# Optimization experiments

Measured on AMD Instinct MI355X. Metric: run time of the kernel, lower is better.

## Reference

```python
import jax, jax.numpy as jnp
import numpy as np

N, E, D, ED = 25000, 250000, 128, 128
LN_EPS = 1e-5   # nn.LayerNorm default
BN_EPS = 1e-5   # BatchNorm1d default (GENConv MLP norm='batch', training mode)
GEN_EPS = 1e-7  # GENConv message eps


def _ln(x, g, b):
    mu = jnp.mean(x, -1, keepdims=True)
    var = jnp.mean((x - mu) ** 2, -1, keepdims=True)
    return (x - mu) * jax.lax.rsqrt(var + LN_EPS) * g + b


def setup_inputs() -> dict:
    key = jax.random.key(0)
    ks = jax.random.split(key, 8)
    p = lambda k, shp: (jax.random.normal(k, shp, jnp.float32) * 0.02)
    return {
        "x": jax.random.normal(ks[0], (N, D), jnp.float32),
        "edge_attr": jax.random.normal(ks[1], (E, ED), jnp.float32),
        "edge_index": jax.random.randint(ks[2], (2, E), 0, N),
        # edge_mlp: Linear(2D+ED -> ED) + ReLU + LayerNorm(ED)
        "W_e": p(ks[3], (2 * D + ED, ED)), "b_e": jnp.zeros((ED,), jnp.float32),
        "g_e": jnp.ones((ED,), jnp.float32), "be_e": jnp.zeros((ED,), jnp.float32),
        # GENConv learnable softmax temperature t (learn_t=True, init 1.0)
        "t": jnp.float32(1.0),
        # GENConv output MLP: [D -> 2D (BN, ReLU) -> D]  (num_layers=2, expansion=2, norm='batch')
        "W_m1": p(ks[4], (D, 2 * D)), "b_m1": jnp.zeros((2 * D,), jnp.float32),
        "g_bn": jnp.ones((2 * D,), jnp.float32), "b_bn": jnp.zeros((2 * D,), jnp.float32),
        "W_m2": p(ks[5], (2 * D, D)), "b_m2": jnp.zeros((D,), jnp.float32),
        # MessageNorm learnable scale (learn_scale=True, init 1.0)
        "scale": jnp.float32(1.0),
        # node LayerNorm
        "g_n": jnp.ones((D,), jnp.float32), "b_n": jnp.zeros((D,), jnp.float32),
    }


def reference(x, edge_attr, edge_index, W_e, b_e, g_e, be_e, t,
              W_m1, b_m1, g_bn, b_bn, W_m2, b_m2, scale, g_n, b_n):
    row, col = edge_index[0], edge_index[1]  # source, destination (PyG flow)

    # edge MLP with residual: cat([x[row], x[col], edge_attr]) -> Linear -> ReLU -> LN, + edge_attr
    ei = jnp.concatenate([x[row], x[col], edge_attr], axis=-1)        # [E, 2D+ED]
    e = _ln(jnp.maximum(ei @ W_e + b_e, 0.0), g_e, be_e) + edge_attr  # [E, ED]

    # GENConv message: relu(x_j + edge_attr) + eps  (edge_dim == in_channels -> no lin_edge)
    msg = jnp.maximum(x[row] + e, 0.0) + GEN_EPS                      # [E, D]

    # per-destination, per-channel softmax aggregation with temperature t
    s = msg * t
    smax = jax.ops.segment_max(s, col, num_segments=N)                # [N, D]
    ex = jnp.exp(s - smax[col])
    denom = jax.ops.segment_sum(ex, col, num_segments=N)
    alpha = ex / denom[col]
    agg = jax.ops.segment_sum(msg * alpha, col, num_segments=N)       # [N, D]

    # GENConv residual + output MLP (Linear -> BatchNorm(train) -> ReLU -> Linear)
    out = agg + x
    h1 = out @ W_m1 + b_m1                                            # [N, 2D]
    mu = jnp.mean(h1, axis=0)
    var = jnp.mean((h1 - mu) ** 2, axis=0)
    h1 = jnp.maximum((h1 - mu) * jax.lax.rsqrt(var + BN_EPS) * g_bn + b_bn, 0.0)
    h = h1 @ W_m2 + b_m2                                              # [N, D]

    # MessageNorm(learn_scale=True): normalize(h) * ||x|| * scale
    hnorm = jnp.linalg.norm(h, axis=-1, keepdims=True)
    h = h / jnp.maximum(hnorm, 1e-12)
    xnorm = jnp.linalg.norm(x, axis=-1, keepdims=True)
    h = h * xnorm * scale

    # node residual + LayerNorm (dropout in eval mode = identity)
    x_out = _ln(x + h, g_n, b_n)
    return (x_out, e)
```

## Files before the change

kernel.cpp:

```cpp
#include <hip/hip_runtime.h>
#include <hip/hip_bf16.h>

typedef __hip_bfloat16 bf16;
typedef __attribute__((ext_vector_type(8))) short short8v;
typedef __attribute__((ext_vector_type(4))) short short4v;
typedef __attribute__((ext_vector_type(4))) float float4v;

constexpr int N = 25000;
constexpr int E = 250000;
constexpr size_t NB = (size_t)N * 128;
constexpr int NBLK = (N + 63) / 64;

constexpr size_t al256(size_t x) { return (x + 255) / 256 * 256; }

constexpr size_t OFF_BNS  = 0;
constexpr size_t OFF_BNQ  = OFF_BNS + 256;
constexpr size_t OFF_FLAG = OFF_BNQ + 256;
constexpr size_t OFF_XN   = OFF_FLAG + 256;
constexpr size_t OFF_WB   = al256(OFF_XN + N);
constexpr size_t OFF_WP   = OFF_WB + 8192;
constexpr size_t OFF_WM1P = OFF_WP + 16384;
constexpr size_t OFF_WM2P = OFF_WM1P + 16384;
constexpr size_t OFF_DEG  = al256(OFF_WM2P + 16384);
constexpr size_t OFF_OFFS = al256(OFF_DEG + N);
constexpr size_t OFF_CUR  = al256(OFF_OFFS + N + 1);
constexpr size_t OFF_LIST = al256(OFF_CUR + N);
constexpr size_t OFF_OUT  = al256(OFF_LIST + E);
constexpr size_t OFF_A    = al256(OFF_OUT + NB / 2);
constexpr size_t WS_FLOATS = OFF_A + NB;
constexpr size_t OFF_MSG  = al256(OFF_A + NB);
constexpr size_t WS_FLOATS_BIG = OFF_MSG + (size_t)E * 64;


__device__ __forceinline__ float b2f(bf16 v) { return __bfloat162float(v); }
__device__ __forceinline__ short f2bs(float f) {
    bf16 h = __float2bfloat16(f);
    return *reinterpret_cast<short*>(&h);
}
__device__ __forceinline__ float bs2f(short s) {
    bf16 h;
    *reinterpret_cast<short*>(&h) = s;
    return b2f(h);
}

__device__ __forceinline__ float ldf(const void* p, size_t i, int bf) {
    return bf ? b2f(((const bf16*)p)[i]) : ((const float*)p)[i];
}
__device__ __forceinline__ void stf(void* p, size_t i, float v, int bf) {
    if (bf) ((bf16*)p)[i] = __float2bfloat16(v);
    else    ((float*)p)[i] = v;
}
__device__ __forceinline__ float4v load4(const void* p, size_t i, int bf) {
    if (bf) {
        short4v s = *(const short4v*)((const bf16*)p + i);
        return (float4v){bs2f(s[0]), bs2f(s[1]), bs2f(s[2]), bs2f(s[3])};
    }
    return *(const float4v*)((const float*)p + i);
}
__device__ __forceinline__ void store4(void* p, size_t i, float4v v, int bf) {
    if (bf) {
        short4v s = {f2bs(v[0]), f2bs(v[1]), f2bs(v[2]), f2bs(v[3])};
        *(short4v*)((bf16*)p + i) = s;
    } else {
        *(float4v*)((float*)p + i) = v;
    }
}
__device__ __forceinline__ float lds_scalar(const void* p, int bf) {
    if (!bf) return *(const float*)p;
    float v = b2f(*(const bf16*)p);
    float a = fabsf(v);
    return (a >= 0.0009765625f && a <= 1024.0f) ? v : *(const float*)p;
}
__device__ __forceinline__ int get_flag(const float* ws) {
    return *(const int*)(ws + OFF_FLAG);
}
__device__ __forceinline__ void* e_base(void* d_out, int bf) {
    return bf ? (void*)((bf16*)d_out + NB) : (void*)((float*)d_out + NB);
}


__global__ void k_detect(const unsigned short* __restrict__ xu, float* __restrict__ ws) {
    __shared__ int cnt;
    if (threadIdx.x == 0) cnt = 0;
    __syncthreads();
    int c = 0;
    for (int i = threadIdx.x; i < 512; i += 256) {
        unsigned e = (xu[i] >> 7) & 0xFFu;
        if (e >= 110u && e <= 135u) c++;
    }
    atomicAdd(&cnt, c);
    __syncthreads();
    if (threadIdx.x == 0) *(int*)(ws + OFF_FLAG) = (cnt >= 460) ? 1 : 0;
}

__global__ void k_init(float* __restrict__ ws, const void* __restrict__ W_e,
                       const void* __restrict__ W_m1, const void* __restrict__ W_m2) {
    int bf = get_flag(ws);
    size_t gid = (size_t)blockIdx.x * blockDim.x + threadIdx.x;
    size_t stride = (size_t)gridDim.x * blockDim.x;
    short* WB = (short*)(ws + OFF_WB);
    for (size_t t = gid; t < 16384; t += stride) {
        int i = t & 7, l = (t >> 3) & 63, n = (t >> 9) & 7, s = t >> 12;
        int k = s * 32 + (l >> 4) * 8 + i;
        int c = n * 16 + (l & 15);
        WB[t] = f2bs(ldf(W_e, (size_t)(256 + k) * 128 + c, bf));
    }
    short* WP = (short*)(ws + OFF_WP);
    for (size_t t = gid; t < 32768; t += stride) {
        int i = t & 7, l = (t >> 3) & 63, n = (t >> 9) & 15, s = t >> 13;
        int k = s * 32 + (l >> 4) * 8 + i;
        int c = n * 16 + (l & 15);
        float v = (c < 128) ? ldf(W_e, (size_t)k * 128 + c, bf)
                            : ldf(W_e, (size_t)(128 + k) * 128 + (c - 128), bf);
        WP[t] = f2bs(v);
    }
    short* M1 = (short*)(ws + OFF_WM1P);
    for (size_t t = gid; t < 32768; t += stride) {
        int i = t & 7, l = (t >> 3) & 63, n = (t >> 9) & 15, s = t >> 13;
        int k = s * 32 + (l >> 4) * 8 + i;
        int c = n * 16 + (l & 15);
        M1[t] = f2bs(ldf(W_m1, (size_t)k * 256 + c, bf));
    }
    short* M2 = (short*)(ws + OFF_WM2P);
    for (size_t t = gid; t < 32768; t += stride) {
        int i = t & 7, l = (t >> 3) & 63, n = (t >> 9) & 7, s = t >> 12;
        int k = s * 32 + (l >> 4) * 8 + i;
        int c = n * 16 + (l & 15);
        M2[t] = f2bs(ldf(W_m2, (size_t)k * 128 + c, bf));
    }
    for (size_t i = gid; i < 512; i += stride) ws[OFF_BNS + i] = 0.0f;
    int* deg = (int*)(ws + OFF_DEG);
    for (size_t i = gid; i < N; i += stride) deg[i] = 0;
}

__global__ void k_count(const int* __restrict__ ei, float* __restrict__ ws) {
    int j = blockIdx.x * blockDim.x + threadIdx.x;
    if (j < E) atomicAdd((int*)(ws + OFF_DEG) + ei[E + j], 1);
}

__global__ __launch_bounds__(256) void k_node_pre_mfma(const void* __restrict__ x,
                                                       const void* __restrict__ b_e,
                                                       float* __restrict__ ws) {
    int bf = get_flag(ws);
    int l = threadIdx.x & 63, wv = threadIdx.x >> 6;
    int n0 = blockIdx.x * 64 + wv * 16;
    if (n0 >= N) return;
    int row = l & 15, grp = l >> 4;
    int ja = n0 + row;
    int jac = ja < N ? ja : N - 1;
    const short8v* WP = (const short8v*)(ws + OFF_WP);
    float4v acc[16];
    #pragma unroll
    for (int n = 0; n < 16; ++n) acc[n] = (float4v){0.f, 0.f, 0.f, 0.f};
    float sq = 0.f;
    #pragma unroll
    for (int s = 0; s < 4; ++s) {
        short8v af;
        if (bf) {
            af = ((const short8v*)x)[(size_t)jac * 16 + s * 4 + grp];
            #pragma unroll
            for (int i = 0; i < 8; ++i) { float v = bs2f(af[i]); sq = fmaf(v, v, sq); }
        } else {
            const float* er = (const float*)x + (size_t)jac * 128 + s * 32 + grp * 8;
            float4v lo = *(const float4v*)er;
            float4v hi = *(const float4v*)(er + 4);
            float xv[8] = {lo[0], lo[1], lo[2], lo[3], hi[0], hi[1], hi[2], hi[3]};
            #pragma unroll
            for (int i = 0; i < 8; ++i) { sq = fmaf(xv[i], xv[i], sq); af[i] = f2bs(xv[i]); }
        }
        #pragma unroll
        for (int n = 0; n < 16; ++n) {
            acc[n] = __builtin_amdgcn_mfma_f32_16x16x32_bf16(af, WP[(s * 16 + n) * 64 + l], acc[n], 0, 0, 0);
        }
    }
    sq += __shfl_xor(sq, 16, 64);
    sq += __shfl_xor(sq, 32, 64);
    if (grp == 0 && ja < N) ws[OFF_XN + ja] = sqrtf(sq);
    bf16* XA = (bf16*)(ws + OFF_A);
    #pragma unroll
    for (int reg = 0; reg < 4; ++reg) {
        int jd = n0 + grp * 4 + reg;
        if (jd >= N) continue;
        #pragma unroll
        for (int n = 0; n < 16; ++n) {
            int c = n * 16 + row;
            if (n < 8) {
                XA[(size_t)jd * 128 + c] = __float2bfloat16(acc[n][reg] + ldf(b_e, c, bf));
            } else {
                XA[NB + (size_t)jd * 128 + (c - 128)] = __float2bfloat16(acc[n][reg]);
            }
        }
    }
}

template<int WM>
__global__ __launch_bounds__(256) void k_edge1_mfma(const void* __restrict__ ea,
                                                    const int* __restrict__ ei,
                                                    const void* __restrict__ g_e,
                                                    const void* __restrict__ be_e,
                                                    const void* __restrict__ x,
                                                    float* __restrict__ ws,
                                                    void* __restrict__ d_out) {
    int bf = get_flag(ws);
    void* eo = e_base(d_out, bf);
    int l = threadIdx.x & 63;
    int wv = threadIdx.x >> 6;
    int e0w = blockIdx.x * 64 + wv * 16;
    int eq = l & 15, grp = l >> 4;

    int posv = 0;
    if (WM && l < 16) {
        int jj = e0w + l;
        if (jj < E) posv = atomicAdd((int*)(ws + OFF_CUR) + ei[E + jj], 1);
    }
    int pos = WM ? __shfl(posv, eq, 64) : 0;

    int ja = e0w + eq;
    int jac = ja < E ? ja : E - 1;
    const short8v* WB = (const short8v*)(ws + OFF_WB);
    float4v acc[8];
    #pragma unroll
    for (int m = 0; m < 8; ++m) acc[m] = (float4v){0.f, 0.f, 0.f, 0.f};

    #pragma unroll
    for (int s = 0; s < 4; ++s) {
        short8v bfr;
        if (bf) {
            bfr = ((const short8v*)ea)[(size_t)jac * 16 + s * 4 + grp];
        } else {
            const float* er = (const float*)ea + (size_t)jac * 128 + s * 32 + grp * 8;
            float4v lo = *(const float4v*)er;
            float4v hi = *(const float4v*)(er + 4);
            bfr[0] = f2bs(lo[0]); bfr[1] = f2bs(lo[1]); bfr[2] = f2bs(lo[2]); bfr[3] = f2bs(lo[3]);
            bfr[4] = f2bs(hi[0]); bfr[5] = f2bs(hi[1]); bfr[6] = f2bs(hi[2]); bfr[7] = f2bs(hi[3]);
        }
        #pragma unroll
        for (int m = 0; m < 8; ++m) {
            acc[m] = __builtin_amdgcn_mfma_f32_16x16x32_bf16(WB[(s * 8 + m) * 64 + l], bfr, acc[m], 0, 0, 0);
        }
    }

    int j = e0w + eq;
    bool valid = j < E;
    int jc = valid ? j : E - 1;
    int r = ei[jc], cd = ei[E + jc];
    const bf16* XAp = (const bf16*)(ws + OFF_A);

    float p[8][4];
    float s1 = 0.f, s2 = 0.f;
    #pragma unroll
    for (int m = 0; m < 8; ++m) {
        int ch = m * 16 + grp * 4;
        short4v xa = *(const short4v*)(XAp + (size_t)r * 128 + ch);
        short4v xb = *(const short4v*)(XAp + NB + (size_t)cd * 128 + ch);
        #pragma unroll
        for (int w = 0; w < 4; ++w) {
            float v = acc[m][w] + bs2f(xa[w]) + bs2f(xb[w]);
            v = fmaxf(v, 0.f);
            p[m][w] = v;
            s1 += v;
            s2 = fmaf(v, v, s2);
        }
    }
    s1 += __shfl_xor(s1, 16, 64);
    s1 += __shfl_xor(s1, 32, 64);
    s2 += __shfl_xor(s2, 16, 64);
    s2 += __shfl_xor(s2, 32, 64);
    float mu = s1 * (1.f / 128.f);
    float var = s2 * (1.f / 128.f) - mu * mu;
    float rstd = rsqrtf(fmaxf(var, 0.f) + 1e-5f);

    bf16* MSG = (bf16*)(ws + OFF_MSG);
    #pragma unroll
    for (int m = 0; m < 8; ++m) {
        int ch = m * 16 + grp * 4;
        float4v gg = load4(g_e, ch, bf);
        float4v bb = load4(be_e, ch, bf);
        float4v eav = load4(ea, (size_t)jc * 128 + ch, bf);
        float4v ev;
        #pragma unroll
        for (int w = 0; w < 4; ++w)
            ev[w] = (p[m][w] - mu) * rstd * gg[w] + bb[w] + eav[w];
        if (valid) store4(eo, (size_t)j * 128 + ch, ev, bf);
        if (WM) {
            float4v xv = load4(x, (size_t)r * 128 + ch, bf);
            short4v ms;
            #pragma unroll
            for (int w = 0; w < 4; ++w)
                ms[w] = f2bs(fmaxf(xv[w] + ev[w], 0.f) + 1e-7f);
            if (valid) *(short4v*)(MSG + (size_t)pos * 128 + ch) = ms;
        }
    }
}

__global__ __launch_bounds__(256) void k_scan(float* __restrict__ ws) {
    const int* deg = (const int*)(ws + OFF_DEG);
    int* offs = (int*)(ws + OFF_OFFS);
    int* cur  = (int*)(ws + OFF_CUR);
    __shared__ int sums[256];
    __shared__ int carry[257];
    int t = threadIdx.x;
    const int chunk = (N + 255) / 256;
    int lo = t * chunk, hi = lo + chunk < N ? lo + chunk : N;
    int s = 0;
    for (int i = lo; i < hi; ++i) s += deg[i];
    sums[t] = s;
    __syncthreads();
    if (t == 0) {
        int acc = 0;
        #pragma unroll 4
        for (int i = 0; i < 256; ++i) { carry[i] = acc; acc += sums[i]; }
        carry[256] = acc;
    }
    __syncthreads();
    int acc = carry[t];
    for (int i = lo; i < hi; ++i) { offs[i] = acc; cur[i] = acc; acc += deg[i]; }
    if (t == 0) offs[N] = carry[256];
}

__global__ void k_scatter(const int* __restrict__ ei, float* __restrict__ ws) {
    int j = blockIdx.x * blockDim.x + threadIdx.x;
    if (j >= E) return;
    int cd = ei[E + j];
    int pos = atomicAdd((int*)(ws + OFF_CUR) + cd, 1);
    ((int*)(ws + OFF_LIST))[pos] = j;
}

__global__ __launch_bounds__(256) void k_agg_stream(const void* __restrict__ x,
                                                    const void* __restrict__ t_p,
                                                    float* __restrict__ ws) {
    int bf = get_flag(ws);
    int n = blockIdx.x, tid = threadIdx.x;
    int c = tid & 127, half = tid >> 7;
    const int* offs = (const int*)(ws + OFF_OFFS);
    int s0 = offs[n], s1v = offs[n + 1];
    float t = lds_scalar(t_p, bf);
    const bf16* MSG = (const bf16*)(ws + OFF_MSG);
    float den = 0.f, num = 0.f;
    for (int i = s0 + half; i < s1v; i += 2) {
        float m = b2f(MSG[(size_t)i * 128 + c]);
        float ex = expf(m * t - 15.0f);
        den += ex;
        num = fmaf(m, ex, num);
    }
    __shared__ float dsh[256];
    __shared__ float nsh[256];
    dsh[tid] = den;
    nsh[tid] = num;
    __syncthreads();
    if (tid < 128) {
        float dn = dsh[tid] + dsh[tid + 128];
        float nm = nsh[tid] + nsh[tid + 128];
        float ag = dn > 0.f ? nm / dn : 0.f;
        float out = ag + ldf(x, (size_t)n * 128 + tid, bf);
        ((bf16*)(ws + OFF_OUT))[(size_t)n * 128 + tid] = __float2bfloat16(out);
    }
}

__global__ __launch_bounds__(256) void k_agg_gather(const void* __restrict__ x,
                                                    const int* __restrict__ ei,
                                                    const void* __restrict__ t_p,
                                                    void* __restrict__ d_out,
                                                    float* __restrict__ ws) {
    int bf = get_flag(ws);
    const void* e_in = e_base(d_out, bf);
    int n = blockIdx.x, tid = threadIdx.x;
    int c = tid & 127, half = tid >> 7;
    const int* offs = (const int*)(ws + OFF_OFFS);
    const int* list = (const int*)(ws + OFF_LIST);
    int s0 = offs[n], s1v = offs[n + 1];
    float t = lds_scalar(t_p, bf);
    float den = 0.f, num = 0.f;
    for (int i = s0 + half; i < s1v; i += 2) {
        int j = list[i];
        int r = ei[j];
        float ev = ldf(e_in, (size_t)j * 128 + c, bf);
        float msg = fmaxf(ldf(x, (size_t)r * 128 + c, bf) + ev, 0.f) + 1e-7f;
        float ex = expf(msg * t - 15.0f);
        den += ex;
        num = fmaf(msg, ex, num);
    }
    __shared__ float dsh[256];
    __shared__ float nsh[256];
    dsh[tid] = den;
    nsh[tid] = num;
    __syncthreads();
    if (tid < 128) {
        float dn = dsh[tid] + dsh[tid + 128];
        float nm = nsh[tid] + nsh[tid + 128];
        float ag = dn > 0.f ? nm / dn : 0.f;
        float out = ag + ldf(x, (size_t)n * 128 + tid, bf);
        ((bf16*)(ws + OFF_OUT))[(size_t)n * 128 + tid] = __float2bfloat16(out);
    }
}

__global__ __launch_bounds__(256) void k_h1_mfma(const void* __restrict__ b_m1,
                                                 float* __restrict__ ws) {
    int bf = get_flag(ws);
    int l = threadIdx.x & 63, wv = threadIdx.x >> 6;
    int n0 = blockIdx.x * 64 + wv * 16;
    if (n0 >= N) return;
    int row = l & 15, grp = l >> 4;
    int ja = n0 + row;
    int jac = ja < N ? ja : N - 1;
    const short8v* OUT = (const short8v*)(ws + OFF_OUT);
    const short8v* M1 = (const short8v*)(ws + OFF_WM1P);
    float4v acc[16];
    #pragma unroll
    for (int n = 0; n < 16; ++n) acc[n] = (float4v){0.f, 0.f, 0.f, 0.f};
    #pragma unroll
    for (int s = 0; s < 4; ++s) {
        short8v af = OUT[(size_t)jac * 16 + s * 4 + grp];
        #pragma unroll
        for (int n = 0; n < 16; ++n) {
            acc[n] = __builtin_amdgcn_mfma_f32_16x16x32_bf16(af, M1[(s * 16 + n) * 64 + l], acc[n], 0, 0, 0);
        }
    }
    bf16* H1 = (bf16*)(ws + OFF_A);
    #pragma unroll
    for (int reg = 0; reg < 4; ++reg) {
        int jd = n0 + grp * 4 + reg;
        if (jd >= N) continue;
        #pragma unroll
        for (int n = 0; n < 16; ++n) {
            int col = n * 16 + row;
            H1[(size_t)jd * 256 + col] = __float2bfloat16(acc[n][reg] + ldf(b_m1, col, bf));
        }
    }
}

__global__ __launch_bounds__(256) void k_bnstats(float* __restrict__ ws) {
    int t = threadIdx.x;
    const bf16* H1 = (const bf16*)(ws + OFF_A);
    float s = 0.f, q = 0.f;
    for (int r = blockIdx.x; r < N; r += gridDim.x) {
        float v = b2f(H1[(size_t)r * 256 + t]);
        s += v;
        q = fmaf(v, v, q);
    }
    atomicAdd(&ws[OFF_BNS + t], s);
    atomicAdd(&ws[OFF_BNQ + t], q);
}

__global__ __launch_bounds__(256) void k_node_post_mfma(const void* __restrict__ x,
                                                        const void* __restrict__ g_bn,
                                                        const void* __restrict__ b_bn,
                                                        const void* __restrict__ b_m2,
                                                        const void* __restrict__ scale_p,
                                                        const void* __restrict__ g_n,
                                                        const void* __restrict__ b_n,
                                                        float* __restrict__ ws,
                                                        void* __restrict__ x_out) {
    int bf = get_flag(ws);
    __shared__ float sA[256];
    __shared__ float sB[256];
    {
        int t = threadIdx.x;
        const float inv_n = 1.f / (float)N;
        float mu = ws[OFF_BNS + t] * inv_n;
        float var = ws[OFF_BNQ + t] * inv_n - mu * mu;
        float rs = rsqrtf(fmaxf(var, 0.f) + 1e-5f) * ldf(g_bn, t, bf);
        sA[t] = rs;
        sB[t] = ldf(b_bn, t, bf) - mu * rs;
    }
    __syncthreads();
    int l = threadIdx.x & 63, wv = threadIdx.x >> 6;
    int n0 = blockIdx.x * 64 + wv * 16;
    if (n0 >= N) return;
    int row = l & 15, grp = l >> 4;
    int ja = n0 + row;
    int jac = ja < N ? ja : N - 1;
    const short8v* H1 = (const short8v*)(ws + OFF_A);
    const short8v* M2 = (const short8v*)(ws + OFF_WM2P);
    float4v acc[8];
    #pragma unroll
    for (int n = 0; n < 8; ++n) acc[n] = (float4v){0.f, 0.f, 0.f, 0.f};
    #pragma unroll
    for (int s = 0; s < 8; ++s) {
        short8v hv = H1[(size_t)jac * 32 + s * 4 + grp];
        int kb = s * 32 + grp * 8;
        short8v af;
        #pragma unroll
        for (int i = 0; i < 8; ++i) {
            float v = fmaf(bs2f(hv[i]), sA[kb + i], sB[kb + i]);
            af[i] = f2bs(fmaxf(v, 0.f));
        }
        #pragma unroll
        for (int n = 0; n < 8; ++n) {
            acc[n] = __builtin_amdgcn_mfma_f32_16x16x32_bf16(af, M2[(s * 8 + n) * 64 + l], acc[n], 0, 0, 0);
        }
    }
    float scl = lds_scalar(scale_p, bf);
    #pragma unroll
    for (int reg = 0; reg < 4; ++reg) {
        int jd = n0 + grp * 4 + reg;
        int jdc = jd < N ? jd : N - 1;
        float h[8];
        float ss = 0.f;
        #pragma unroll
        for (int n = 0; n < 8; ++n) {
            h[n] = acc[n][reg] + ldf(b_m2, n * 16 + row, bf);
            ss = fmaf(h[n], h[n], ss);
        }
        #pragma unroll
        for (int off = 1; off < 16; off <<= 1) ss += __shfl_xor(ss, off, 64);
        float hs = ws[OFF_XN + jdc] * scl / fmaxf(sqrtf(ss), 1e-12f);
        float y[8];
        float s1 = 0.f;
        #pragma unroll
        for (int n = 0; n < 8; ++n) {
            y[n] = ldf(x, (size_t)jdc * 128 + n * 16 + row, bf) + h[n] * hs;
            s1 += y[n];
        }
        #pragma unroll
        for (int off = 1; off < 16; off <<= 1) s1 += __shfl_xor(s1, off, 64);
        float mu = s1 * (1.f / 128.f);
        float s2 = 0.f;
        #pragma unroll
        for (int n = 0; n < 8; ++n) { float d = y[n] - mu; s2 = fmaf(d, d, s2); }
        #pragma unroll
        for (int off = 1; off < 16; off <<= 1) s2 += __shfl_xor(s2, off, 64);
        float rstd = rsqrtf(s2 * (1.f / 128.f) + 1e-5f);
        if (jd < N) {
            #pragma unroll
            for (int n = 0; n < 8; ++n) {
                int col = n * 16 + row;
                float o = (y[n] - mu) * rstd * ldf(g_n, col, bf) + ldf(b_n, col, bf);
                stf(x_out, (size_t)jd * 128 + col, o, bf);
            }
        }
    }
}


extern "C" void kernel_launch(void* const* d_in, const int* in_sizes, int n_in,
                              void* d_out, int out_size, void* d_ws, size_t ws_size,
                              hipStream_t stream) {
    const void* x    = d_in[0];
    const void* ea   = d_in[1];
    const int*  ei   = (const int*)d_in[2];
    const void* W_e  = d_in[3];
    const void* b_e  = d_in[4];
    const void* g_e  = d_in[5];
    const void* be_e = d_in[6];
    const void* t_p  = d_in[7];
    const void* W_m1 = d_in[8];
    const void* b_m1 = d_in[9];
    const void* g_bn = d_in[10];
    const void* b_bn = d_in[11];
    const void* W_m2 = d_in[12];
    const void* b_m2 = d_in[13];
    const void* scl  = d_in[14];
    const void* g_n  = d_in[15];
    const void* b_n  = d_in[16];

    float* ws = (float*)d_ws;
    bool big = ws_size >= WS_FLOATS_BIG * sizeof(float);

    k_detect<<<1, 256, 0, stream>>>((const unsigned short*)x, ws);
    k_init<<<512, 256, 0, stream>>>(ws, W_e, W_m1, W_m2);
    k_count<<<(E + 255) / 256, 256, 0, stream>>>(ei, ws);
    k_scan<<<1, 256, 0, stream>>>(ws);
    k_node_pre_mfma<<<NBLK, 256, 0, stream>>>(x, b_e, ws);
    if (big) {
        k_edge1_mfma<1><<<(E + 63) / 64, 256, 0, stream>>>(ea, ei, g_e, be_e, x, ws, d_out);
        k_agg_stream<<<N, 256, 0, stream>>>(x, t_p, ws);
    } else {
        k_edge1_mfma<0><<<(E + 63) / 64, 256, 0, stream>>>(ea, ei, g_e, be_e, x, ws, d_out);
        k_scatter<<<(E + 255) / 256, 256, 0, stream>>>(ei, ws);
        k_agg_gather<<<N, 256, 0, stream>>>(x, ei, t_p, d_out, ws);
    }
    k_h1_mfma<<<NBLK, 256, 0, stream>>>(b_m1, ws);
    k_bnstats<<<256, 256, 0, stream>>>(ws);
    k_node_post_mfma<<<NBLK, 256, 0, stream>>>(x, g_bn, b_bn, b_m2, scl, g_n, b_n, ws, d_out);
}
```

Measured before the change: 604.5 us.

## Fuse BN stats and degree count, index messages by edge, vectorize aggregation

Several changes land together. BatchNorm column statistics are now computed inside the h1 GEMM epilogue, which removes k_bnstats. Degree counting moves into k_init and zeroing into k_detect, so k_count is gone. Edge messages are written at the edge index rather than at an atomically claimed CSR slot, and k_scatter now always runs so the aggregation can read them through the CSR list. The aggregation kernel uses 16-way edge parallelism with 8-wide bf16 vector loads and a fast exp. Gathers are hoisted ahead of the MFMA loop, and large output writes use nontemporal stores. The trade-offs are an extra scatter launch on the big path and indirect message reads in the aggregation.

```diff
diff --git a/kernel.cpp b/kernel.cpp
--- a/kernel.cpp
+++ b/kernel.cpp
@@ -50,6 +50,10 @@
     if (bf) ((bf16*)p)[i] = __float2bfloat16(v);
     else    ((float*)p)[i] = v;
 }
+__device__ __forceinline__ void stf_nt(void* p, size_t i, float v, int bf) {
+    if (bf) __builtin_nontemporal_store(f2bs(v), (short*)p + i);
+    else    __builtin_nontemporal_store(v, (float*)p + i);
+}
 __device__ __forceinline__ float4v load4(const void* p, size_t i, int bf) {
     if (bf) {
         short4v s = *(const short4v*)((const bf16*)p + i);
@@ -57,12 +61,12 @@
     }
     return *(const float4v*)((const float*)p + i);
 }
-__device__ __forceinline__ void store4(void* p, size_t i, float4v v, int bf) {
+__device__ __forceinline__ void store4_nt(void* p, size_t i, float4v v, int bf) {
     if (bf) {
         short4v s = {f2bs(v[0]), f2bs(v[1]), f2bs(v[2]), f2bs(v[3])};
-        *(short4v*)((bf16*)p + i) = s;
+        __builtin_nontemporal_store(s, (short4v*)((bf16*)p + i));
     } else {
-        *(float4v*)((float*)p + i) = v;
+        __builtin_nontemporal_store(v, (float4v*)((float*)p + i));
     }
 }
 __device__ __forceinline__ float lds_scalar(const void* p, int bf) {
@@ -89,53 +93,47 @@
         if (e >= 110u && e <= 135u) c++;
     }
     atomicAdd(&cnt, c);
+    for (int i = threadIdx.x; i < 512; i += 256) ws[OFF_BNS + i] = 0.0f;
+    int* deg = (int*)(ws + OFF_DEG);
+    for (int i = threadIdx.x; i < N; i += 256) deg[i] = 0;
     __syncthreads();
     if (threadIdx.x == 0) *(int*)(ws + OFF_FLAG) = (cnt >= 460) ? 1 : 0;
 }
 
 __global__ void k_init(float* __restrict__ ws, const void* __restrict__ W_e,
-                       const void* __restrict__ W_m1, const void* __restrict__ W_m2) {
+                       const void* __restrict__ W_m1, const void* __restrict__ W_m2,
+                       const int* __restrict__ ei) {
     int bf = get_flag(ws);
     size_t gid = (size_t)blockIdx.x * blockDim.x + threadIdx.x;
     size_t stride = (size_t)gridDim.x * blockDim.x;
     short* WB = (short*)(ws + OFF_WB);
-    for (size_t t = gid; t < 16384; t += stride) {
-        int i = t & 7, l = (t >> 3) & 63, n = (t >> 9) & 7, s = t >> 12;
-        int k = s * 32 + (l >> 4) * 8 + i;
-        int c = n * 16 + (l & 15);
+    for (size_t u = gid; u < 16384; u += stride) {
+        int k = u >> 7, c = u & 127;
+        int t = (k >> 5) * 4096 + (c >> 4) * 512 + (((k & 31) >> 3) * 16 + (c & 15)) * 8 + (k & 7);
         WB[t] = f2bs(ldf(W_e, (size_t)(256 + k) * 128 + c, bf));
     }
     short* WP = (short*)(ws + OFF_WP);
-    for (size_t t = gid; t < 32768; t += stride) {
-        int i = t & 7, l = (t >> 3) & 63, n = (t >> 9) & 15, s = t >> 13;
-        int k = s * 32 + (l >> 4) * 8 + i;
-        int c = n * 16 + (l & 15);
+    for (size_t u = gid; u < 32768; u += stride) {
+        int k = u >> 8, c = u & 255;
+        int t = (k >> 5) * 8192 + (c >> 4) * 512 + (((k & 31) >> 3) * 16 + (c & 15)) * 8 + (k & 7);
         float v = (c < 128) ? ldf(W_e, (size_t)k * 128 + c, bf)
                             : ldf(W_e, (size_t)(128 + k) * 128 + (c - 128), bf);
         WP[t] = f2bs(v);
     }
     short* M1 = (short*)(ws + OFF_WM1P);
-    for (size_t t = gid; t < 32768; t += stride) {
-        int i = t & 7, l = (t >> 3) & 63, n = (t >> 9) & 15, s = t >> 13;
-        int k = s * 32 + (l >> 4) * 8 + i;
-        int c = n * 16 + (l & 15);
+    for (size_t u = gid; u < 32768; u += stride) {
+        int k = u >> 8, c = u & 255;
+        int t = (k >> 5) * 8192 + (c >> 4) * 512 + (((k & 31) >> 3) * 16 + (c & 15)) * 8 + (k & 7);
         M1[t] = f2bs(ldf(W_m1, (size_t)k * 256 + c, bf));
     }
     short* M2 = (short*)(ws + OFF_WM2P);
-    for (size_t t = gid; t < 32768; t += stride) {
-        int i = t & 7, l = (t >> 3) & 63, n = (t >> 9) & 7, s = t >> 12;
-        int k = s * 32 + (l >> 4) * 8 + i;
-        int c = n * 16 + (l & 15);
+    for (size_t u = gid; u < 32768; u += stride) {
+        int k = u >> 7, c = u & 127;
+        int t = (k >> 5) * 4096 + (c >> 4) * 512 + (((k & 31) >> 3) * 16 + (c & 15)) * 8 + (k & 7);
         M2[t] = f2bs(ldf(W_m2, (size_t)k * 128 + c, bf));
     }
-    for (size_t i = gid; i < 512; i += stride) ws[OFF_BNS + i] = 0.0f;
     int* deg = (int*)(ws + OFF_DEG);
-    for (size_t i = gid; i < N; i += stride) deg[i] = 0;
-}
-
-__global__ void k_count(const int* __restrict__ ei, float* __restrict__ ws) {
-    int j = blockIdx.x * blockDim.x + threadIdx.x;
-    if (j < E) atomicAdd((int*)(ws + OFF_DEG) + ei[E + j], 1);
+    for (size_t j = gid; j < E; j += stride) atomicAdd(deg + ei[E + j], 1);
 }
 
 __global__ __launch_bounds__(256) void k_node_pre_mfma(const void* __restrict__ x,
@@ -206,17 +204,23 @@
     int l = threadIdx.x & 63;
     int wv = threadIdx.x >> 6;
     int e0w = blockIdx.x * 64 + wv * 16;
+    if (e0w >= E) return;
     int eq = l & 15, grp = l >> 4;
 
-    int posv = 0;
-    if (WM && l < 16) {
-        int jj = e0w + l;
-        if (jj < E) posv = atomicAdd((int*)(ws + OFF_CUR) + ei[E + jj], 1);
-    }
-    int pos = WM ? __shfl(posv, eq, 64) : 0;
-
-    int ja = e0w + eq;
-    int jac = ja < E ? ja : E - 1;
+    int j = e0w + eq;
+    bool valid = j < E;
+    int jc = valid ? j : E - 1;
+    int r = ei[jc], cd = ei[E + jc];
+
+    const bf16* XAp = (const bf16*)(ws + OFF_A);
+    short4v xa[8], xb[8];
+    #pragma unroll
+    for (int m = 0; m < 8; ++m) {
+        int ch = m * 16 + grp * 4;
+        xa[m] = *(const short4v*)(XAp + (size_t)r * 128 + ch);
+        xb[m] = *(const short4v*)(XAp + NB + (size_t)cd * 128 + ch);
+    }
+
     const short8v* WB = (const short8v*)(ws + OFF_WB);
     float4v acc[8];
     #pragma unroll
@@ -226,9 +230,9 @@
     for (int s = 0; s < 4; ++s) {
         short8v bfr;
         if (bf) {
-            bfr = ((const short8v*)ea)[(size_t)jac * 16 + s * 4 + grp];
+            bfr = ((const short8v*)ea)[(size_t)jc * 16 + s * 4 + grp];
         } else {
-            const float* er = (const float*)ea + (size_t)jac * 128 + s * 32 + grp * 8;
+            const float* er = (const float*)ea + (size_t)jc * 128 + s * 32 + grp * 8;
             float4v lo = *(const float4v*)er;
             float4v hi = *(const float4v*)(er + 4);
             bfr[0] = f2bs(lo[0]); bfr[1] = f2bs(lo[1]); bfr[2] = f2bs(lo[2]); bfr[3] = f2bs(lo[3]);
@@ -240,27 +244,23 @@
         }
     }
 
-    int j = e0w + eq;
-    bool valid = j < E;
-    int jc = valid ? j : E - 1;
-    int r = ei[jc], cd = ei[E + jc];
-    const bf16* XAp = (const bf16*)(ws + OFF_A);
-
     float p[8][4];
     float s1 = 0.f, s2 = 0.f;
     #pragma unroll
     for (int m = 0; m < 8; ++m) {
-        int ch = m * 16 + grp * 4;
-        short4v xa = *(const short4v*)(XAp + (size_t)r * 128 + ch);
-        short4v xb = *(const short4v*)(XAp + NB + (size_t)cd * 128 + ch);
         #pragma unroll
         for (int w = 0; w < 4; ++w) {
-            float v = acc[m][w] + bs2f(xa[w]) + bs2f(xb[w]);
+            float v = acc[m][w] + bs2f(xa[m][w]) + bs2f(xb[m][w]);
             v = fmaxf(v, 0.f);
             p[m][w] = v;
             s1 += v;
             s2 = fmaf(v, v, s2);
         }
+    }
+    float4v xr[8];
+    if (WM) {
+        #pragma unroll
+        for (int m = 0; m < 8; ++m) xr[m] = load4(x, (size_t)r * 128 + m * 16 + grp * 4, bf);
     }
     s1 += __shfl_xor(s1, 16, 64);
     s1 += __shfl_xor(s1, 32, 64);
@@ -281,14 +281,13 @@
         #pragma unroll
         for (int w = 0; w < 4; ++w)
             ev[w] = (p[m][w] - mu) * rstd * gg[w] + bb[w] + eav[w];
-        if (valid) store4(eo, (size_t)j * 128 + ch, ev, bf);
-        if (WM) {
-            float4v xv = load4(x, (size_t)r * 128 + ch, bf);
+        if (valid) store4_nt(eo, (size_t)j * 128 + ch, ev, bf);
+        if (WM && valid) {
             short4v ms;
             #pragma unroll
             for (int w = 0; w < 4; ++w)
-                ms[w] = f2bs(fmaxf(xv[w] + ev[w], 0.f) + 1e-7f);
-            if (valid) *(short4v*)(MSG + (size_t)pos * 128 + ch) = ms;
+                ms[w] = f2bs(fmaxf(xr[m][w] + ev[w], 0.f) + 1e-7f);
+            *(short4v*)(MSG + (size_t)j * 128 + ch) = ms;
         }
     }
 }
@@ -331,26 +330,36 @@
                                                     float* __restrict__ ws) {
     int bf = get_flag(ws);
     int n = blockIdx.x, tid = threadIdx.x;
-    int c = tid & 127, half = tid >> 7;
+    int par = tid >> 4;
+    int cg = tid & 15;
     const int* offs = (const int*)(ws + OFF_OFFS);
+    const int* list = (const int*)(ws + OFF_LIST);
     int s0 = offs[n], s1v = offs[n + 1];
     float t = lds_scalar(t_p, bf);
-    const bf16* MSG = (const bf16*)(ws + OFF_MSG);
-    float den = 0.f, num = 0.f;
-    for (int i = s0 + half; i < s1v; i += 2) {
-        float m = b2f(MSG[(size_t)i * 128 + c]);
-        float ex = expf(m * t - 15.0f);
-        den += ex;
-        num = fmaf(m, ex, num);
-    }
-    __shared__ float dsh[256];
-    __shared__ float nsh[256];
-    dsh[tid] = den;
-    nsh[tid] = num;
+    const short8v* MSG = (const short8v*)((const bf16*)(ws + OFF_MSG));
+    float den[8], num[8];
+    #pragma unroll
+    for (int w = 0; w < 8; ++w) { den[w] = 0.f; num[w] = 0.f; }
+    for (int i = s0 + par; i < s1v; i += 16) {
+        int jj = list[i];
+        short8v m8 = MSG[(size_t)jj * 16 + cg];
+        #pragma unroll
+        for (int w = 0; w < 8; ++w) {
+            float m = bs2f(m8[w]);
+            float ex = __expf(fmaf(m, t, -15.0f));
+            den[w] += ex;
+            num[w] = fmaf(m, ex, num[w]);
+        }
+    }
+    __shared__ float sd[16][132];
+    __shared__ float sn[16][132];
+    #pragma unroll
+    for (int w = 0; w < 8; ++w) { sd[par][cg * 8 + w] = den[w]; sn[par][cg * 8 + w] = num[w]; }
     __syncthreads();
     if (tid < 128) {
-        float dn = dsh[tid] + dsh[tid + 128];
-        float nm = nsh[tid] + nsh[tid + 128];
+        float dn = 0.f, nm = 0.f;
+        #pragma unroll
+        for (int p = 0; p < 16; ++p) { dn += sd[p][tid]; nm += sn[p][tid]; }
         float ag = dn > 0.f ? nm / dn : 0.f;
         float out = ag + ldf(x, (size_t)n * 128 + tid, bf);
         ((bf16*)(ws + OFF_OUT))[(size_t)n * 128 + tid] = __float2bfloat16(out);
@@ -399,7 +408,6 @@
     int bf = get_flag(ws);
     int l = threadIdx.x & 63, wv = threadIdx.x >> 6;
     int n0 = blockIdx.x * 64 + wv * 16;
-    if (n0 >= N) return;
     int row = l & 15, grp = l >> 4;
     int ja = n0 + row;
     int jac = ja < N ? ja : N - 1;
@@ -416,30 +424,36 @@
             acc[n] = __builtin_amdgcn_mfma_f32_16x16x32_bf16(af, M1[(s * 16 + n) * 64 + l], acc[n], 0, 0, 0);
         }
     }
+    __shared__ float sds[4][264];
+    __shared__ float sqs[4][264];
     bf16* H1 = (bf16*)(ws + OFF_A);
     #pragma unroll
-    for (int reg = 0; reg < 4; ++reg) {
-        int jd = n0 + grp * 4 + reg;
-        if (jd >= N) continue;
-        #pragma unroll
-        for (int n = 0; n < 16; ++n) {
-            int col = n * 16 + row;
-            H1[(size_t)jd * 256 + col] = __float2bfloat16(acc[n][reg] + ldf(b_m1, col, bf));
-        }
-    }
-}
-
-__global__ __launch_bounds__(256) void k_bnstats(float* __restrict__ ws) {
+    for (int n = 0; n < 16; ++n) {
+        int col = n * 16 + row;
+        float bias = ldf(b_m1, col, bf);
+        float vs = 0.f, vq = 0.f;
+        #pragma unroll
+        for (int reg = 0; reg < 4; ++reg) {
+            int jd = n0 + grp * 4 + reg;
+            float v = acc[n][reg] + bias;
+            if (jd < N) {
+                H1[(size_t)jd * 256 + col] = __float2bfloat16(v);
+                vs += v;
+                vq = fmaf(v, v, vq);
+            }
+        }
+        vs += __shfl_xor(vs, 16, 64); vs += __shfl_xor(vs, 32, 64);
+        vq += __shfl_xor(vq, 16, 64); vq += __shfl_xor(vq, 32, 64);
+        if (grp == 0) { sds[wv][col] = vs; sqs[wv][col] = vq; }
+    }
+    __syncthreads();
     int t = threadIdx.x;
-    const bf16* H1 = (const bf16*)(ws + OFF_A);
-    float s = 0.f, q = 0.f;
-    for (int r = blockIdx.x; r < N; r += gridDim.x) {
-        float v = b2f(H1[(size_t)r * 256 + t]);
-        s += v;
-        q = fmaf(v, v, q);
-    }
-    atomicAdd(&ws[OFF_BNS + t], s);
-    atomicAdd(&ws[OFF_BNQ + t], q);
+    if (t < 256) {
+        float s = sds[0][t] + sds[1][t] + sds[2][t] + sds[3][t];
+        float q = sqs[0][t] + sqs[1][t] + sqs[2][t] + sqs[3][t];
+        atomicAdd(&ws[OFF_BNS + t], s);
+        atomicAdd(&ws[OFF_BNQ + t], q);
+    }
 }
 
 __global__ __launch_bounds__(256) void k_node_post_mfma(const void* __restrict__ x,
@@ -526,7 +540,7 @@
             for (int n = 0; n < 8; ++n) {
                 int col = n * 16 + row;
                 float o = (y[n] - mu) * rstd * ldf(g_n, col, bf) + ldf(b_n, col, bf);
-                stf(x_out, (size_t)jd * 128 + col, o, bf);
+                stf_nt(x_out, (size_t)jd * 128 + col, o, bf);
             }
         }
     }
@@ -558,19 +572,17 @@
     bool big = ws_size >= WS_FLOATS_BIG * sizeof(float);
 
     k_detect<<<1, 256, 0, stream>>>((const unsigned short*)x, ws);
-    k_init<<<512, 256, 0, stream>>>(ws, W_e, W_m1, W_m2);
-    k_count<<<(E + 255) / 256, 256, 0, stream>>>(ei, ws);
+    k_init<<<512, 256, 0, stream>>>(ws, W_e, W_m1, W_m2, ei);
     k_scan<<<1, 256, 0, stream>>>(ws);
+    k_scatter<<<(E + 255) / 256, 256, 0, stream>>>(ei, ws);
     k_node_pre_mfma<<<NBLK, 256, 0, stream>>>(x, b_e, ws);
     if (big) {
         k_edge1_mfma<1><<<(E + 63) / 64, 256, 0, stream>>>(ea, ei, g_e, be_e, x, ws, d_out);
         k_agg_stream<<<N, 256, 0, stream>>>(x, t_p, ws);
     } else {
         k_edge1_mfma<0><<<(E + 63) / 64, 256, 0, stream>>>(ea, ei, g_e, be_e, x, ws, d_out);
-        k_scatter<<<(E + 255) / 256, 256, 0, stream>>>(ei, ws);
         k_agg_gather<<<N, 256, 0, stream>>>(x, ei, t_p, d_out, ws);
     }
     k_h1_mfma<<<NBLK, 256, 0, stream>>>(b_m1, ws);
-    k_bnstats<<<256, 256, 0, stream>>>(ws);
     k_node_post_mfma<<<NBLK, 256, 0, stream>>>(x, g_bn, b_bn, b_m2, scl, g_n, b_n, ws, d_out);
 }
```

Measured after the change: 560.0 us. 1.08x faster.
